# Performance work log

Measured on AMD Instinct MI355X. Metric: run time of the kernel, lower is better.

Reference implementation:

```python
import jax, jax.numpy as jnp
import numpy as np
import math

B, H, S, D = 1, 16, 2048, 64

def setup_inputs() -> dict:
    key = jax.random.key(0)
    kq, kk, kv = jax.random.split(key, 3)
    return {
        "query_tensor": jax.random.normal(kq, (B, H, S, D), dtype=jnp.float32),
        "key_tensor": jax.random.normal(kk, (B, H, S, D), dtype=jnp.float32),
        "value_tensor": jax.random.normal(kv, (B, H, S, D), dtype=jnp.float32),
    }

def reference(query_tensor, key_tensor, value_tensor):
    d_k = key_tensor.shape[-1]
    # scores: [B, H, S, S]
    scores = jnp.einsum("bhqd,bhkd->bhqk", query_tensor, key_tensor) / math.sqrt(d_k)
    attn = jax.nn.softmax(scores, axis=-1)
    context = jnp.einsum("bhqk,bhkd->bhqd", attn, value_tensor)
    return context, attn
```

## Files before the change

kernel.cpp:

```cpp
#include <hip/hip_runtime.h>
#include <math.h>

#define S 2048
#define D 64
#define H 16
#define BR 64
#define BC 64
#define NIT (S / BC)
#define KSTR 72

typedef __attribute__((ext_vector_type(8))) short bf16x8;
typedef __attribute__((ext_vector_type(4))) float f32x4;

__device__ __forceinline__ unsigned short f2bf(float x) {
    unsigned u = __float_as_uint(x);
    u += 0x7fffu + ((u >> 16) & 1u);
    return (unsigned short)(u >> 16);
}
__device__ __forceinline__ float bf2f(unsigned short h) {
    return __uint_as_float(((unsigned)h) << 16);
}

#define LGKM0() asm volatile("s_waitcnt lgkmcnt(0)" ::: "memory")
#define BAR()   __builtin_amdgcn_s_barrier()

__global__ __launch_bounds__(256, 2)
void k_attn_fused(const float* __restrict__ Q, const float* __restrict__ K,
                  const float* __restrict__ V, float* __restrict__ ctx,
                  float* __restrict__ attn) {
    __shared__ __align__(16) unsigned short Qs[BR * KSTR];
    __shared__ __align__(16) unsigned short Ks[BC * KSTR];
    __shared__ __align__(16) unsigned short Vthi[D * KSTR];
    __shared__ __align__(16) unsigned short Vtlo[D * KSTR];
    __shared__ __align__(16) unsigned short Phi[BR * KSTR];
    __shared__ __align__(16) unsigned short Plo[BR * KSTR];

    const int h  = blockIdx.y;
    const int r0 = blockIdx.x * BR;
    const int t  = threadIdx.x;
    const int w    = t >> 6;
    const int lane = t & 63;
    const int l16  = lane & 15;
    const int quad = lane >> 4;

    const float* Qh = Q + (size_t)h * S * D;
    const float* Kh = K + (size_t)h * S * D;
    const float* Vh = V + (size_t)h * S * D;

#pragma unroll
    for (int p = 0; p < 4; ++p) {
        int idx = t + p * 256;
        int r = idx >> 4, c4 = (idx & 15) * 4;
        float4 v = *(const float4*)(Qh + (size_t)(r0 + r) * D + c4);
        *(ushort4*)&Qs[r * KSTR + c4] =
            make_ushort4(f2bf(v.x), f2bf(v.y), f2bf(v.z), f2bf(v.w));
    }
    LGKM0(); BAR();

    bf16x8 bq[2];
    bq[0] = *(const bf16x8*)&Qs[(w * 16 + l16) * KSTR + 0 * 32 + quad * 8];
    bq[1] = *(const bf16x8*)&Qs[(w * 16 + l16) * KSTR + 1 * 32 + quad * 8];

    const f32x4 zero4 = {0.f, 0.f, 0.f, 0.f};
    float lsum = 0.f;

    float4 kreg[4];
#pragma unroll
    for (int p = 0; p < 4; ++p) {
        int idx = t + p * 256;
        int r = idx >> 4, c4 = (idx & 15) * 4;
        kreg[p] = *(const float4*)(Kh + (size_t)r * D + c4);
    }
    for (int kt = 0; kt < NIT; ++kt) {
#pragma unroll
        for (int p = 0; p < 4; ++p) {
            int idx = t + p * 256;
            int r = idx >> 4, c4 = (idx & 15) * 4;
            *(ushort4*)&Ks[r * KSTR + c4] =
                make_ushort4(f2bf(kreg[p].x), f2bf(kreg[p].y), f2bf(kreg[p].z), f2bf(kreg[p].w));
        }
        LGKM0(); BAR();
        if (kt + 1 < NIT) {
#pragma unroll
            for (int p = 0; p < 4; ++p) {
                int idx = t + p * 256;
                int r = idx >> 4, c4 = (idx & 15) * 4;
                kreg[p] = *(const float4*)(Kh + (size_t)((kt + 1) * BC + r) * D + c4);
            }
        }
        f32x4 acc[4] = {zero4, zero4, zero4, zero4};
#pragma unroll
        for (int ks = 0; ks < 2; ++ks)
#pragma unroll
            for (int cs = 0; cs < 4; ++cs) {
                bf16x8 ak = *(const bf16x8*)&Ks[(cs * 16 + l16) * KSTR + ks * 32 + quad * 8];
                acc[cs] = __builtin_amdgcn_mfma_f32_16x16x32_bf16(ak, bq[ks], acc[cs], 0, 0, 0);
            }
        float e = 0.f;
#pragma unroll
        for (int cs = 0; cs < 4; ++cs)
#pragma unroll
            for (int r2 = 0; r2 < 4; ++r2)
                e += __expf(acc[cs][r2] * 0.125f);
        e += __shfl_xor(e, 16);
        e += __shfl_xor(e, 32);
        lsum += e;
        BAR();
    }
    const float linv = 1.0f / lsum;

    f32x4 cacc[4] = {zero4, zero4, zero4, zero4};
    float4 vreg[4];
#pragma unroll
    for (int p = 0; p < 4; ++p) {
        int idx = t + p * 256;
        int r = idx >> 4, c4 = (idx & 15) * 4;
        kreg[p] = *(const float4*)(Kh + (size_t)r * D + c4);
        vreg[p] = *(const float4*)(Vh + (size_t)r * D + c4);
    }
    for (int kt = 0; kt < NIT; ++kt) {
#pragma unroll
        for (int p = 0; p < 4; ++p) {
            int idx = t + p * 256;
            int r = idx >> 4, c4 = (idx & 15) * 4;
            *(ushort4*)&Ks[r * KSTR + c4] =
                make_ushort4(f2bf(kreg[p].x), f2bf(kreg[p].y), f2bf(kreg[p].z), f2bf(kreg[p].w));
            float vv[4] = {vreg[p].x, vreg[p].y, vreg[p].z, vreg[p].w};
#pragma unroll
            for (int c = 0; c < 4; ++c) {
                unsigned short hi = f2bf(vv[c]);
                Vthi[(c4 + c) * KSTR + r] = hi;
                Vtlo[(c4 + c) * KSTR + r] = f2bf(vv[c] - bf2f(hi));
            }
        }
        LGKM0(); BAR();
        if (kt + 1 < NIT) {
#pragma unroll
            for (int p = 0; p < 4; ++p) {
                int idx = t + p * 256;
                int r = idx >> 4, c4 = (idx & 15) * 4;
                kreg[p] = *(const float4*)(Kh + (size_t)((kt + 1) * BC + r) * D + c4);
                vreg[p] = *(const float4*)(Vh + (size_t)((kt + 1) * BC + r) * D + c4);
            }
        }
        f32x4 acc[4] = {zero4, zero4, zero4, zero4};
#pragma unroll
        for (int ks = 0; ks < 2; ++ks)
#pragma unroll
            for (int cs = 0; cs < 4; ++cs) {
                bf16x8 ak = *(const bf16x8*)&Ks[(cs * 16 + l16) * KSTR + ks * 32 + quad * 8];
                acc[cs] = __builtin_amdgcn_mfma_f32_16x16x32_bf16(ak, bq[ks], acc[cs], 0, 0, 0);
            }

        float* arow = attn + (size_t)(h * S + r0 + w * 16 + l16) * S + (size_t)kt * BC;
        const int prow = (w * 16 + l16) * KSTR;
#pragma unroll
        for (int cs = 0; cs < 4; ++cs) {
            f32x4 pv;
#pragma unroll
            for (int r2 = 0; r2 < 4; ++r2)
                pv[r2] = __expf(acc[cs][r2] * 0.125f) * linv;
            __builtin_nontemporal_store(pv, (f32x4*)(arow + cs * 16 + quad * 4));
            unsigned short h0 = f2bf(pv[0]), h1 = f2bf(pv[1]),
                           h2 = f2bf(pv[2]), h3 = f2bf(pv[3]);
            *(ushort4*)&Phi[prow + cs * 16 + quad * 4] = make_ushort4(h0, h1, h2, h3);
            *(ushort4*)&Plo[prow + cs * 16 + quad * 4] =
                make_ushort4(f2bf(pv[0] - bf2f(h0)), f2bf(pv[1] - bf2f(h1)),
                             f2bf(pv[2] - bf2f(h2)), f2bf(pv[3] - bf2f(h3)));
        }
        asm volatile("" ::: "memory");

#pragma unroll
        for (int ks = 0; ks < 2; ++ks) {
            bf16x8 ah = *(const bf16x8*)&Phi[prow + ks * 32 + quad * 8];
            bf16x8 al = *(const bf16x8*)&Plo[prow + ks * 32 + quad * 8];
#pragma unroll
            for (int vs = 0; vs < 4; ++vs) {
                bf16x8 bh = *(const bf16x8*)&Vthi[(vs * 16 + l16) * KSTR + ks * 32 + quad * 8];
                bf16x8 bl = *(const bf16x8*)&Vtlo[(vs * 16 + l16) * KSTR + ks * 32 + quad * 8];
                cacc[vs] = __builtin_amdgcn_mfma_f32_16x16x32_bf16(bh, ah, cacc[vs], 0, 0, 0);
                cacc[vs] = __builtin_amdgcn_mfma_f32_16x16x32_bf16(bl, ah, cacc[vs], 0, 0, 0);
                cacc[vs] = __builtin_amdgcn_mfma_f32_16x16x32_bf16(bh, al, cacc[vs], 0, 0, 0);
            }
        }
        BAR();
    }

    float* crow = ctx + (size_t)(h * S + r0 + w * 16 + l16) * D;
#pragma unroll
    for (int vs = 0; vs < 4; ++vs)
        *(f32x4*)(crow + vs * 16 + quad * 4) = cacc[vs];
}

extern "C" void kernel_launch(void* const* d_in, const int* in_sizes, int n_in,
                              void* d_out, int out_size, void* d_ws, size_t ws_size,
                              hipStream_t stream) {
    (void)in_sizes; (void)n_in; (void)d_ws; (void)ws_size; (void)out_size;
    const float* Q = (const float*)d_in[0];
    const float* K = (const float*)d_in[1];
    const float* V = (const float*)d_in[2];
    float* ctx  = (float*)d_out;
    float* attn = (float*)d_out + (size_t)H * S * D;

    k_attn_fused<<<dim3(S / BR, H), 256, 0, stream>>>(Q, K, V, ctx, attn);
}
```

Measured before the change: 412.8 us.

## Store V row-major in blocked LDS layout and read it with transpose loads

Replaces the scalar transposed V stores into LDS (eight 2-byte scattered writes per element group) with vectorized ushort4 stores into a blocked row-major layout. The PV matmul operands are then fetched with ds_read_b64_tr_b16 transpose reads using hard-coded offsets. The change also flattens the grid to 1D and remaps block IDs so heads interleave across blocks, which may spread work differently across XCDs or caches. It risks correctness if the blocked offsets and transpose-read semantics do not match the MFMA operand layout.

```diff
diff --git a/kernel.cpp b/kernel.cpp
--- a/kernel.cpp
+++ b/kernel.cpp
@@ -9,7 +9,12 @@
 #define NIT (S / BC)
 #define KSTR 72
 
+#define VT_SUB  72
+#define VT_DBLK 1184
+#define VT_SIZE (4 * VT_DBLK)
+
 typedef __attribute__((ext_vector_type(8))) short bf16x8;
+typedef __attribute__((ext_vector_type(4))) short bf16x4;
 typedef __attribute__((ext_vector_type(4))) float f32x4;
 
 __device__ __forceinline__ unsigned short f2bf(float x) {
@@ -23,6 +28,42 @@
 
 #define LGKM0() asm volatile("s_waitcnt lgkmcnt(0)" ::: "memory")
 #define BAR()   __builtin_amdgcn_s_barrier()
+
+template <int OFF>
+__device__ __forceinline__ bf16x4 tr_read(unsigned addr) {
+    bf16x4 d;
+    asm volatile("ds_read_b64_tr_b16 %0, %1 offset:%c2"
+                 : "=v"(d) : "v"(addr), "i"(OFF));
+    return d;
+}
+
+template <int KS>
+__device__ __forceinline__ void pv_step(const unsigned short* Phi_,
+                                        const unsigned short* Plo_,
+                                        int prow, int quad,
+                                        unsigned a_hi, unsigned a_lo,
+                                        f32x4* cacc) {
+    bf16x8 ah = *(const bf16x8*)&Phi_[prow + KS * 32 + quad * 8];
+    bf16x8 al = *(const bf16x8*)&Plo_[prow + KS * 32 + quad * 8];
+    bf16x4 th[8], tl[8];
+#define TRPAIR(vs) \
+    th[2*(vs)]   = tr_read<KS*1152 + (vs)*2368 +   0>(a_hi); \
+    th[2*(vs)+1] = tr_read<KS*1152 + (vs)*2368 + 144>(a_hi); \
+    tl[2*(vs)]   = tr_read<KS*1152 + (vs)*2368 +   0>(a_lo); \
+    tl[2*(vs)+1] = tr_read<KS*1152 + (vs)*2368 + 144>(a_lo);
+    TRPAIR(0) TRPAIR(1) TRPAIR(2) TRPAIR(3)
+#undef TRPAIR
+    LGKM0();
+    __builtin_amdgcn_sched_barrier(0);
+#pragma unroll
+    for (int vs = 0; vs < 4; ++vs) {
+        bf16x8 bh = __builtin_shufflevector(th[2*vs], th[2*vs+1], 0,1,2,3,4,5,6,7);
+        bf16x8 bl = __builtin_shufflevector(tl[2*vs], tl[2*vs+1], 0,1,2,3,4,5,6,7);
+        cacc[vs] = __builtin_amdgcn_mfma_f32_16x16x32_bf16(bh, ah, cacc[vs], 0, 0, 0);
+        cacc[vs] = __builtin_amdgcn_mfma_f32_16x16x32_bf16(bl, ah, cacc[vs], 0, 0, 0);
+        cacc[vs] = __builtin_amdgcn_mfma_f32_16x16x32_bf16(bh, al, cacc[vs], 0, 0, 0);
+    }
+}
 
 __global__ __launch_bounds__(256, 2)
 void k_attn_fused(const float* __restrict__ Q, const float* __restrict__ K,
@@ -30,13 +71,16 @@
                   float* __restrict__ attn) {
     __shared__ __align__(16) unsigned short Qs[BR * KSTR];
     __shared__ __align__(16) unsigned short Ks[BC * KSTR];
-    __shared__ __align__(16) unsigned short Vthi[D * KSTR];
-    __shared__ __align__(16) unsigned short Vtlo[D * KSTR];
+    __shared__ __align__(16) unsigned short Vthi[VT_SIZE];
+    __shared__ __align__(16) unsigned short Vtlo[VT_SIZE];
     __shared__ __align__(16) unsigned short Phi[BR * KSTR];
     __shared__ __align__(16) unsigned short Plo[BR * KSTR];
 
-    const int h  = blockIdx.y;
-    const int r0 = blockIdx.x * BR;
+    const int bid = blockIdx.x;
+    const int idx_in = bid >> 3;
+    const int h  = ((bid & 7) << 1) | (idx_in >> 5);
+    const int r0 = (idx_in & 31) * BR;
+
     const int t  = threadIdx.x;
     const int w    = t >> 6;
     const int lane = t & 63;
@@ -46,6 +90,10 @@
     const float* Qh = Q + (size_t)h * S * D;
     const float* Kh = K + (size_t)h * S * D;
     const float* Vh = V + (size_t)h * S * D;
+
+    const unsigned lpart = (unsigned)(quad * 288 + l16 * 8);
+    const unsigned a_vhi = (unsigned)(uintptr_t)&Vthi[0] + lpart;
+    const unsigned a_vlo = (unsigned)(uintptr_t)&Vtlo[0] + lpart;
 
 #pragma unroll
     for (int p = 0; p < 4; ++p) {
@@ -125,13 +173,13 @@
             int r = idx >> 4, c4 = (idx & 15) * 4;
             *(ushort4*)&Ks[r * KSTR + c4] =
                 make_ushort4(f2bf(kreg[p].x), f2bf(kreg[p].y), f2bf(kreg[p].z), f2bf(kreg[p].w));
-            float vv[4] = {vreg[p].x, vreg[p].y, vreg[p].z, vreg[p].w};
-#pragma unroll
-            for (int c = 0; c < 4; ++c) {
-                unsigned short hi = f2bf(vv[c]);
-                Vthi[(c4 + c) * KSTR + r] = hi;
-                Vtlo[(c4 + c) * KSTR + r] = f2bf(vv[c] - bf2f(hi));
-            }
+            unsigned short h0 = f2bf(vreg[p].x), h1 = f2bf(vreg[p].y),
+                           h2 = f2bf(vreg[p].z), h3 = f2bf(vreg[p].w);
+            int vtoff = (c4 >> 4) * VT_DBLK + (r >> 2) * VT_SUB + (r & 3) * 16 + (c4 & 15);
+            *(ushort4*)&Vthi[vtoff] = make_ushort4(h0, h1, h2, h3);
+            *(ushort4*)&Vtlo[vtoff] =
+                make_ushort4(f2bf(vreg[p].x - bf2f(h0)), f2bf(vreg[p].y - bf2f(h1)),
+                             f2bf(vreg[p].z - bf2f(h2)), f2bf(vreg[p].w - bf2f(h3)));
         }
         LGKM0(); BAR();
         if (kt + 1 < NIT) {
@@ -170,20 +218,11 @@
         }
         asm volatile("" ::: "memory");
 
-#pragma unroll
-        for (int ks = 0; ks < 2; ++ks) {
-            bf16x8 ah = *(const bf16x8*)&Phi[prow + ks * 32 + quad * 8];
-            bf16x8 al = *(const bf16x8*)&Plo[prow + ks * 32 + quad * 8];
-#pragma unroll
-            for (int vs = 0; vs < 4; ++vs) {
-                bf16x8 bh = *(const bf16x8*)&Vthi[(vs * 16 + l16) * KSTR + ks * 32 + quad * 8];
-                bf16x8 bl = *(const bf16x8*)&Vtlo[(vs * 16 + l16) * KSTR + ks * 32 + quad * 8];
-                cacc[vs] = __builtin_amdgcn_mfma_f32_16x16x32_bf16(bh, ah, cacc[vs], 0, 0, 0);
-                cacc[vs] = __builtin_amdgcn_mfma_f32_16x16x32_bf16(bl, ah, cacc[vs], 0, 0, 0);
-                cacc[vs] = __builtin_amdgcn_mfma_f32_16x16x32_bf16(bh, al, cacc[vs], 0, 0, 0);
-            }
-        }
+        pv_step<0>(Phi, Plo, prow, quad, a_vhi, a_vlo, cacc);
+        pv_step<1>(Phi, Plo, prow, quad, a_vhi, a_vlo, cacc);
+
         BAR();
+        asm volatile("" ::: "memory");
     }
 
     float* crow = ctx + (size_t)(h * S + r0 + w * 16 + l16) * D;
@@ -202,5 +241,5 @@
     float* ctx  = (float*)d_out;
     float* attn = (float*)d_out + (size_t)H * S * D;
 
-    k_attn_fused<<<dim3(S / BR, H), 256, 0, stream>>>(Q, K, V, ctx, attn);
-}
+    k_attn_fused<<<dim3((S / BR) * H), 256, 0, stream>>>(Q, K, V, ctx, attn);
+}
```

Result: slower. 443.2 us (+7.4%).

## Stage attn tiles through LDS for coalesced stores; transpose V via lane loads; remap blocks

Applied to the files above, without the earlier changes.

Each 16-row by 32-column half of the probability tile is staged in LDS, reusing the Q buffer, so that each lane writes contiguous 128-byte row segments to the attn output instead of scattered 16-byte pieces. V is now loaded with one column per lane, which lets the transposed hi/lo bf16 copies be written as ushort4 vectors with a padded stride instead of scalar 2-byte stores. The grid is flattened and remapped so that consecutive blocks spread across heads, likely to balance per-XCD locality. The change adds LDS traffic and reuses Qs space, which is safe only because bq was already read into registers. The staging reads from As have no barrier, which relies on each wave touching only its own rows.

```diff
diff --git a/kernel.cpp b/kernel.cpp
--- a/kernel.cpp
+++ b/kernel.cpp
@@ -8,6 +8,8 @@
 #define BC 64
 #define NIT (S / BC)
 #define KSTR 72
+#define VSTR 88
+#define ASTR 36
 
 typedef __attribute__((ext_vector_type(8))) short bf16x8;
 typedef __attribute__((ext_vector_type(4))) float f32x4;
@@ -30,13 +32,17 @@
                   float* __restrict__ attn) {
     __shared__ __align__(16) unsigned short Qs[BR * KSTR];
     __shared__ __align__(16) unsigned short Ks[BC * KSTR];
-    __shared__ __align__(16) unsigned short Vthi[D * KSTR];
-    __shared__ __align__(16) unsigned short Vtlo[D * KSTR];
+    __shared__ __align__(16) unsigned short Vthi[D * VSTR];
+    __shared__ __align__(16) unsigned short Vtlo[D * VSTR];
     __shared__ __align__(16) unsigned short Phi[BR * KSTR];
     __shared__ __align__(16) unsigned short Plo[BR * KSTR];
-
-    const int h  = blockIdx.y;
-    const int r0 = blockIdx.x * BR;
+    float* As = (float*)Qs;
+
+    const int bid = blockIdx.x;
+    const int idx_in = bid >> 3;
+    const int h  = ((bid & 7) << 1) | (idx_in >> 5);
+    const int r0 = (idx_in & 31) * BR;
+
     const int t  = threadIdx.x;
     const int w    = t >> 6;
     const int lane = t & 63;
@@ -110,13 +116,15 @@
     const float linv = 1.0f / lsum;
 
     f32x4 cacc[4] = {zero4, zero4, zero4, zero4};
-    float4 vreg[4];
+    float vr[16];
 #pragma unroll
     for (int p = 0; p < 4; ++p) {
         int idx = t + p * 256;
         int r = idx >> 4, c4 = (idx & 15) * 4;
         kreg[p] = *(const float4*)(Kh + (size_t)r * D + c4);
-        vreg[p] = *(const float4*)(Vh + (size_t)r * D + c4);
+#pragma unroll
+        for (int i = 0; i < 4; ++i)
+            vr[p * 4 + i] = Vh[(size_t)(w * 16 + p * 4 + i) * D + lane];
     }
     for (int kt = 0; kt < NIT; ++kt) {
 #pragma unroll
@@ -125,13 +133,13 @@
             int r = idx >> 4, c4 = (idx & 15) * 4;
             *(ushort4*)&Ks[r * KSTR + c4] =
                 make_ushort4(f2bf(kreg[p].x), f2bf(kreg[p].y), f2bf(kreg[p].z), f2bf(kreg[p].w));
-            float vv[4] = {vreg[p].x, vreg[p].y, vreg[p].z, vreg[p].w};
-#pragma unroll
-            for (int c = 0; c < 4; ++c) {
-                unsigned short hi = f2bf(vv[c]);
-                Vthi[(c4 + c) * KSTR + r] = hi;
-                Vtlo[(c4 + c) * KSTR + r] = f2bf(vv[c] - bf2f(hi));
-            }
+            const int kb = w * 16 + p * 4;
+            unsigned short h0 = f2bf(vr[p * 4 + 0]), h1 = f2bf(vr[p * 4 + 1]),
+                           h2 = f2bf(vr[p * 4 + 2]), h3 = f2bf(vr[p * 4 + 3]);
+            *(ushort4*)&Vthi[lane * VSTR + kb] = make_ushort4(h0, h1, h2, h3);
+            *(ushort4*)&Vtlo[lane * VSTR + kb] =
+                make_ushort4(f2bf(vr[p * 4 + 0] - bf2f(h0)), f2bf(vr[p * 4 + 1] - bf2f(h1)),
+                             f2bf(vr[p * 4 + 2] - bf2f(h2)), f2bf(vr[p * 4 + 3] - bf2f(h3)));
         }
         LGKM0(); BAR();
         if (kt + 1 < NIT) {
@@ -140,7 +148,9 @@
                 int idx = t + p * 256;
                 int r = idx >> 4, c4 = (idx & 15) * 4;
                 kreg[p] = *(const float4*)(Kh + (size_t)((kt + 1) * BC + r) * D + c4);
-                vreg[p] = *(const float4*)(Vh + (size_t)((kt + 1) * BC + r) * D + c4);
+#pragma unroll
+                for (int i = 0; i < 4; ++i)
+                    vr[p * 4 + i] = Vh[(size_t)((kt + 1) * BC + w * 16 + p * 4 + i) * D + lane];
             }
         }
         f32x4 acc[4] = {zero4, zero4, zero4, zero4};
@@ -152,23 +162,33 @@
                 acc[cs] = __builtin_amdgcn_mfma_f32_16x16x32_bf16(ak, bq[ks], acc[cs], 0, 0, 0);
             }
 
-        float* arow = attn + (size_t)(h * S + r0 + w * 16 + l16) * S + (size_t)kt * BC;
         const int prow = (w * 16 + l16) * KSTR;
 #pragma unroll
-        for (int cs = 0; cs < 4; ++cs) {
-            f32x4 pv;
-#pragma unroll
-            for (int r2 = 0; r2 < 4; ++r2)
-                pv[r2] = __expf(acc[cs][r2] * 0.125f) * linv;
-            __builtin_nontemporal_store(pv, (f32x4*)(arow + cs * 16 + quad * 4));
-            unsigned short h0 = f2bf(pv[0]), h1 = f2bf(pv[1]),
-                           h2 = f2bf(pv[2]), h3 = f2bf(pv[3]);
-            *(ushort4*)&Phi[prow + cs * 16 + quad * 4] = make_ushort4(h0, h1, h2, h3);
-            *(ushort4*)&Plo[prow + cs * 16 + quad * 4] =
-                make_ushort4(f2bf(pv[0] - bf2f(h0)), f2bf(pv[1] - bf2f(h1)),
-                             f2bf(pv[2] - bf2f(h2)), f2bf(pv[3] - bf2f(h3)));
-        }
-        asm volatile("" ::: "memory");
+        for (int half = 0; half < 2; ++half) {
+#pragma unroll
+            for (int csr = 0; csr < 2; ++csr) {
+                const int cs = half * 2 + csr;
+                f32x4 pv;
+#pragma unroll
+                for (int r2 = 0; r2 < 4; ++r2)
+                    pv[r2] = __expf(acc[cs][r2] * 0.125f) * linv;
+                *(f32x4*)&As[(w * 16 + l16) * ASTR + csr * 16 + quad * 4] = pv;
+                unsigned short h0 = f2bf(pv[0]), h1 = f2bf(pv[1]),
+                               h2 = f2bf(pv[2]), h3 = f2bf(pv[3]);
+                *(ushort4*)&Phi[prow + cs * 16 + quad * 4] = make_ushort4(h0, h1, h2, h3);
+                *(ushort4*)&Plo[prow + cs * 16 + quad * 4] =
+                    make_ushort4(f2bf(pv[0] - bf2f(h0)), f2bf(pv[1] - bf2f(h1)),
+                                 f2bf(pv[2] - bf2f(h2)), f2bf(pv[3] - bf2f(h3)));
+            }
+#pragma unroll
+            for (int i = 0; i < 2; ++i) {
+                const int row = w * 16 + (lane >> 3) + 8 * i;
+                f32x4 tv = *(const f32x4*)&As[row * ASTR + (lane & 7) * 4];
+                __builtin_nontemporal_store(
+                    tv, (f32x4*)(attn + (size_t)(h * S + r0 + row) * S +
+                                 (size_t)kt * BC + half * 32 + (lane & 7) * 4));
+            }
+        }
 
 #pragma unroll
         for (int ks = 0; ks < 2; ++ks) {
@@ -176,8 +196,8 @@
             bf16x8 al = *(const bf16x8*)&Plo[prow + ks * 32 + quad * 8];
 #pragma unroll
             for (int vs = 0; vs < 4; ++vs) {
-                bf16x8 bh = *(const bf16x8*)&Vthi[(vs * 16 + l16) * KSTR + ks * 32 + quad * 8];
-                bf16x8 bl = *(const bf16x8*)&Vtlo[(vs * 16 + l16) * KSTR + ks * 32 + quad * 8];
+                bf16x8 bh = *(const bf16x8*)&Vthi[(vs * 16 + l16) * VSTR + ks * 32 + quad * 8];
+                bf16x8 bl = *(const bf16x8*)&Vtlo[(vs * 16 + l16) * VSTR + ks * 32 + quad * 8];
                 cacc[vs] = __builtin_amdgcn_mfma_f32_16x16x32_bf16(bh, ah, cacc[vs], 0, 0, 0);
                 cacc[vs] = __builtin_amdgcn_mfma_f32_16x16x32_bf16(bl, ah, cacc[vs], 0, 0, 0);
                 cacc[vs] = __builtin_amdgcn_mfma_f32_16x16x32_bf16(bh, al, cacc[vs], 0, 0, 0);
@@ -202,5 +222,5 @@
     float* ctx  = (float*)d_out;
     float* attn = (float*)d_out + (size_t)H * S * D;
 
-    k_attn_fused<<<dim3(S / BR, H), 256, 0, stream>>>(Q, K, V, ctx, attn);
-}
+    k_attn_fused<<<dim3((S / BR) * H), 256, 0, stream>>>(Q, K, V, ctx, attn);
+}
```

Result: faster. 376.7 us (-8.7%).

## Double-buffer K/V shared tiles, remap blocks across heads, pack bf16 conversions

Applied to the files above, without the earlier changes.

K and V tiles are now double-buffered in LDS and staged into the next buffer right after the QK MFMAs, so one barrier per iteration replaces two and global loads are issued two tiles ahead. V is loaded per-column and written transposed with a padded stride to reduce LDS bank conflicts. The P tile reuses the Q buffer. The grid is flattened with a swizzled head/row mapping. bf16 conversion now uses packed hardware-style float2 conversion. The extra buffers raise LDS use, which risks lowering occupancy, and the per-element V loads are narrower global accesses.

```diff
diff --git a/kernel.cpp b/kernel.cpp
--- a/kernel.cpp
+++ b/kernel.cpp
@@ -1,4 +1,5 @@
 #include <hip/hip_runtime.h>
+#include <hip/hip_bf16.h>
 #include <math.h>
 
 #define S 2048
@@ -8,17 +9,16 @@
 #define BC 64
 #define NIT (S / BC)
 #define KSTR 72
+#define VSTR 84
 
 typedef __attribute__((ext_vector_type(8))) short bf16x8;
+typedef __attribute__((ext_vector_type(4))) short bf16x4;
 typedef __attribute__((ext_vector_type(4))) float f32x4;
 
-__device__ __forceinline__ unsigned short f2bf(float x) {
-    unsigned u = __float_as_uint(x);
-    u += 0x7fffu + ((u >> 16) & 1u);
-    return (unsigned short)(u >> 16);
-}
-__device__ __forceinline__ float bf2f(unsigned short h) {
-    return __uint_as_float(((unsigned)h) << 16);
+__device__ __forceinline__ unsigned pk2(float a, float b) {
+    __hip_bfloat162 h2 = __float22bfloat162_rn(make_float2(a, b));
+    unsigned u; __builtin_memcpy(&u, &h2, 4);
+    return u;
 }
 
 #define LGKM0() asm volatile("s_waitcnt lgkmcnt(0)" ::: "memory")
@@ -29,31 +29,72 @@
                   const float* __restrict__ V, float* __restrict__ ctx,
                   float* __restrict__ attn) {
     __shared__ __align__(16) unsigned short Qs[BR * KSTR];
-    __shared__ __align__(16) unsigned short Ks[BC * KSTR];
-    __shared__ __align__(16) unsigned short Vthi[D * KSTR];
-    __shared__ __align__(16) unsigned short Vtlo[D * KSTR];
-    __shared__ __align__(16) unsigned short Phi[BR * KSTR];
+    __shared__ __align__(16) unsigned short Ks[2][BC * KSTR];
+    __shared__ __align__(16) unsigned short Vthi[2][D * VSTR];
+    __shared__ __align__(16) unsigned short Vtlo[2][D * VSTR];
     __shared__ __align__(16) unsigned short Plo[BR * KSTR];
-
-    const int h  = blockIdx.y;
-    const int r0 = blockIdx.x * BR;
+    unsigned short* Phi = Qs;
+
+    const int bid = blockIdx.x;
+    const int idx_in = bid >> 3;
+    const int h  = ((bid & 7) << 1) | (idx_in >> 5);
+    const int r0 = (idx_in & 31) * BR;
+
     const int t  = threadIdx.x;
     const int w    = t >> 6;
     const int lane = t & 63;
     const int l16  = lane & 15;
     const int quad = lane >> 4;
+    const int rb   = t >> 4;
+    const int c4   = (t & 15) * 4;
 
     const float* Qh = Q + (size_t)h * S * D;
     const float* Kh = K + (size_t)h * S * D;
     const float* Vh = V + (size_t)h * S * D;
 
+    float4 kreg[4];
+    float  vr[16];
+
+    auto loadK = [&](int tile) {
+#pragma unroll
+        for (int p = 0; p < 4; ++p)
+            kreg[p] = *(const float4*)(Kh + ((size_t)tile * BC + rb + p * 16) * D + c4);
+    };
+    auto loadV = [&](int tile) {
+#pragma unroll
+        for (int p = 0; p < 4; ++p)
+#pragma unroll
+            for (int i = 0; i < 4; ++i)
+                vr[p * 4 + i] = Vh[((size_t)tile * BC + w * 16 + p * 4 + i) * D + lane];
+    };
+    auto stageK = [&](int buf) {
+#pragma unroll
+        for (int p = 0; p < 4; ++p) {
+            int r = rb + p * 16;
+            *(uint2*)&Ks[buf][r * KSTR + c4] =
+                make_uint2(pk2(kreg[p].x, kreg[p].y), pk2(kreg[p].z, kreg[p].w));
+        }
+    };
+    auto stageV = [&](int buf) {
+#pragma unroll
+        for (int p = 0; p < 4; ++p) {
+            const int kb = w * 16 + p * 4;
+            unsigned uh01 = pk2(vr[p * 4 + 0], vr[p * 4 + 1]);
+            unsigned uh23 = pk2(vr[p * 4 + 2], vr[p * 4 + 3]);
+            *(uint2*)&Vthi[buf][lane * VSTR + kb] = make_uint2(uh01, uh23);
+            float l0 = vr[p * 4 + 0] - __uint_as_float(uh01 << 16);
+            float l1 = vr[p * 4 + 1] - __uint_as_float(uh01 & 0xffff0000u);
+            float l2 = vr[p * 4 + 2] - __uint_as_float(uh23 << 16);
+            float l3 = vr[p * 4 + 3] - __uint_as_float(uh23 & 0xffff0000u);
+            *(uint2*)&Vtlo[buf][lane * VSTR + kb] = make_uint2(pk2(l0, l1), pk2(l2, l3));
+        }
+    };
+
 #pragma unroll
     for (int p = 0; p < 4; ++p) {
-        int idx = t + p * 256;
-        int r = idx >> 4, c4 = (idx & 15) * 4;
+        int r = rb + p * 16;
         float4 v = *(const float4*)(Qh + (size_t)(r0 + r) * D + c4);
-        *(ushort4*)&Qs[r * KSTR + c4] =
-            make_ushort4(f2bf(v.x), f2bf(v.y), f2bf(v.z), f2bf(v.w));
+        *(uint2*)&Qs[r * KSTR + c4] = make_uint2(pk2(v.x, v.y), pk2(v.z, v.w));
     }
     LGKM0(); BAR();
 
@@ -64,38 +105,22 @@
     const f32x4 zero4 = {0.f, 0.f, 0.f, 0.f};
     float lsum = 0.f;
 
-    float4 kreg[4];
-#pragma unroll
-    for (int p = 0; p < 4; ++p) {
-        int idx = t + p * 256;
-        int r = idx >> 4, c4 = (idx & 15) * 4;
-        kreg[p] = *(const float4*)(Kh + (size_t)r * D + c4);
-    }
+    loadK(0);
+    stageK(0);
+    loadK(1);
     for (int kt = 0; kt < NIT; ++kt) {
-#pragma unroll
-        for (int p = 0; p < 4; ++p) {
-            int idx = t + p * 256;
-            int r = idx >> 4, c4 = (idx & 15) * 4;
-            *(ushort4*)&Ks[r * KSTR + c4] =
-                make_ushort4(f2bf(kreg[p].x), f2bf(kreg[p].y), f2bf(kreg[p].z), f2bf(kreg[p].w));
-        }
+        const int cur = kt & 1;
         LGKM0(); BAR();
-        if (kt + 1 < NIT) {
-#pragma unroll
-            for (int p = 0; p < 4; ++p) {
-                int idx = t + p * 256;
-                int r = idx >> 4, c4 = (idx & 15) * 4;
-                kreg[p] = *(const float4*)(Kh + (size_t)((kt + 1) * BC + r) * D + c4);
-            }
-        }
         f32x4 acc[4] = {zero4, zero4, zero4, zero4};
 #pragma unroll
         for (int ks = 0; ks < 2; ++ks)
 #pragma unroll
             for (int cs = 0; cs < 4; ++cs) {
-                bf16x8 ak = *(const bf16x8*)&Ks[(cs * 16 + l16) * KSTR + ks * 32 + quad * 8];
+                bf16x8 ak = *(const bf16x8*)&Ks[cur][(cs * 16 + l16) * KSTR + ks * 32 + quad * 8];
                 acc[cs] = __builtin_amdgcn_mfma_f32_16x16x32_bf16(ak, bq[ks], acc[cs], 0, 0, 0);
             }
+        if (kt + 1 < NIT) stageK(cur ^ 1);
+        if (kt + 2 < NIT) loadK(kt + 2);
         float e = 0.f;
 #pragma unroll
         for (int cs = 0; cs < 4; ++cs)
@@ -105,55 +130,29 @@
         e += __shfl_xor(e, 16);
         e += __shfl_xor(e, 32);
         lsum += e;
-        BAR();
     }
     const float linv = 1.0f / lsum;
 
     f32x4 cacc[4] = {zero4, zero4, zero4, zero4};
-    float4 vreg[4];
-#pragma unroll
-    for (int p = 0; p < 4; ++p) {
-        int idx = t + p * 256;
-        int r = idx >> 4, c4 = (idx & 15) * 4;
-        kreg[p] = *(const float4*)(Kh + (size_t)r * D + c4);
-        vreg[p] = *(const float4*)(Vh + (size_t)r * D + c4);
-    }
+    loadK(0); loadV(0);
+    stageK(0); stageV(0);
+    loadK(1); loadV(1);
     for (int kt = 0; kt < NIT; ++kt) {
-#pragma unroll
-        for (int p = 0; p < 4; ++p) {
-            int idx = t + p * 256;
-            int r = idx >> 4, c4 = (idx & 15) * 4;
-            *(ushort4*)&Ks[r * KSTR + c4] =
-                make_ushort4(f2bf(kreg[p].x), f2bf(kreg[p].y), f2bf(kreg[p].z), f2bf(kreg[p].w));
-            float vv[4] = {vreg[p].x, vreg[p].y, vreg[p].z, vreg[p].w};
-#pragma unroll
-            for (int c = 0; c < 4; ++c) {
-                unsigned short hi = f2bf(vv[c]);
-                Vthi[(c4 + c) * KSTR + r] = hi;
-                Vtlo[(c4 + c) * KSTR + r] = f2bf(vv[c] - bf2f(hi));
-            }
-        }
+        const int cur = kt & 1;
         LGKM0(); BAR();
-        if (kt + 1 < NIT) {
-#pragma unroll
-            for (int p = 0; p < 4; ++p) {
-                int idx = t + p * 256;
-                int r = idx >> 4, c4 = (idx & 15) * 4;
-                kreg[p] = *(const float4*)(Kh + (size_t)((kt + 1) * BC + r) * D + c4);
-                vreg[p] = *(const float4*)(Vh + (size_t)((kt + 1) * BC + r) * D + c4);
-            }
-        }
         f32x4 acc[4] = {zero4, zero4, zero4, zero4};
 #pragma unroll
         for (int ks = 0; ks < 2; ++ks)
 #pragma unroll
             for (int cs = 0; cs < 4; ++cs) {
-                bf16x8 ak = *(const bf16x8*)&Ks[(cs * 16 + l16) * KSTR + ks * 32 + quad * 8];
+                bf16x8 ak = *(const bf16x8*)&Ks[cur][(cs * 16 + l16) * KSTR + ks * 32 + quad * 8];
                 acc[cs] = __builtin_amdgcn_mfma_f32_16x16x32_bf16(ak, bq[ks], acc[cs], 0, 0, 0);
             }
-
+        if (kt + 1 < NIT) { stageK(cur ^ 1); stageV(cur ^ 1); }
+        if (kt + 2 < NIT) { loadK(kt + 2); loadV(kt + 2); }
+
+        const int prow = (w * 16 + l16) * KSTR;
         float* arow = attn + (size_t)(h * S + r0 + w * 16 + l16) * S + (size_t)kt * BC;
-        const int prow = (w * 16 + l16) * KSTR;
 #pragma unroll
         for (int cs = 0; cs < 4; ++cs) {
             f32x4 pv;
@@ -161,14 +160,15 @@
             for (int r2 = 0; r2 < 4; ++r2)
                 pv[r2] = __expf(acc[cs][r2] * 0.125f) * linv;
             __builtin_nontemporal_store(pv, (f32x4*)(arow + cs * 16 + quad * 4));
-            unsigned short h0 = f2bf(pv[0]), h1 = f2bf(pv[1]),
-                           h2 = f2bf(pv[2]), h3 = f2bf(pv[3]);
-            *(ushort4*)&Phi[prow + cs * 16 + quad * 4] = make_ushort4(h0, h1, h2, h3);
-            *(ushort4*)&Plo[prow + cs * 16 + quad * 4] =
-                make_ushort4(f2bf(pv[0] - bf2f(h0)), f2bf(pv[1] - bf2f(h1)),
-                             f2bf(pv[2] - bf2f(h2)), f2bf(pv[3] - bf2f(h3)));
-        }
-        asm volatile("" ::: "memory");
+            unsigned uh01 = pk2(pv[0], pv[1]);
+            unsigned uh23 = pk2(pv[2], pv[3]);
+            *(uint2*)&Phi[prow + cs * 16 + quad * 4] = make_uint2(uh01, uh23);
+            float l0 = pv[0] - __uint_as_float(uh01 << 16);
+            float l1 = pv[1] - __uint_as_float(uh01 & 0xffff0000u);
+            float l2 = pv[2] - __uint_as_float(uh23 << 16);
+            float l3 = pv[3] - __uint_as_float(uh23 & 0xffff0000u);
+            *(uint2*)&Plo[prow + cs * 16 + quad * 4] = make_uint2(pk2(l0, l1), pk2(l2, l3));
+        }
 
 #pragma unroll
         for (int ks = 0; ks < 2; ++ks) {
@@ -176,14 +176,18 @@
             bf16x8 al = *(const bf16x8*)&Plo[prow + ks * 32 + quad * 8];
 #pragma unroll
             for (int vs = 0; vs < 4; ++vs) {
-                bf16x8 bh = *(const bf16x8*)&Vthi[(vs * 16 + l16) * KSTR + ks * 32 + quad * 8];
-                bf16x8 bl = *(const bf16x8*)&Vtlo[(vs * 16 + l16) * KSTR + ks * 32 + quad * 8];
+                const int vo = (vs * 16 + l16) * VSTR + ks * 32 + quad * 8;
+                bf16x4 h0 = *(const bf16x4*)&Vthi[cur][vo];
+                bf16x4 h1 = *(const bf16x4*)&Vthi[cur][vo + 4];
+                bf16x4 g0 = *(const bf16x4*)&Vtlo[cur][vo];
+                bf16x4 g1 = *(const bf16x4*)&Vtlo[cur][vo + 4];
+                bf16x8 bh = __builtin_shufflevector(h0, h1, 0, 1, 2, 3, 4, 5, 6, 7);
+                bf16x8 bl = __builtin_shufflevector(g0, g1, 0, 1, 2, 3, 4, 5, 6, 7);
                 cacc[vs] = __builtin_amdgcn_mfma_f32_16x16x32_bf16(bh, ah, cacc[vs], 0, 0, 0);
                 cacc[vs] = __builtin_amdgcn_mfma_f32_16x16x32_bf16(bl, ah, cacc[vs], 0, 0, 0);
                 cacc[vs] = __builtin_amdgcn_mfma_f32_16x16x32_bf16(bh, al, cacc[vs], 0, 0, 0);
             }
         }
-        BAR();
     }
 
     float* crow = ctx + (size_t)(h * S + r0 + w * 16 + l16) * D;
@@ -202,5 +206,5 @@
     float* ctx  = (float*)d_out;
     float* attn = (float*)d_out + (size_t)H * S * D;
 
-    k_attn_fused<<<dim3(S / BR, H), 256, 0, stream>>>(Q, K, V, ctx, attn);
+    k_attn_fused<<<dim3((S / BR) * H), 256, 0, stream>>>(Q, K, V, ctx, attn);
 }
```

Result: faster. 388.1 us (-6.0%).
